# Optimization experiments

Measured on AMD Instinct MI355X. Metric: run time of the kernel, lower is better.

## Reference

```python
import jax, jax.numpy as jnp
import numpy as np

B, S0, S1 = 4, 768, 256
T = S0 + S1
D0, D1 = 2048, 1024
N, K, H = 8, 1, 256  # num_heads, num_kv_heads, head_dim
G = N // K
BIG_NEG = -2.3819763e38


def _apply_rope(x, positions, max_wavelength=10000):
    # x: [B, L, Hn, Hd]; positions: [B, L] float32
    half = x.shape[-1] // 2
    freq_exponents = (2.0 / x.shape[-1]) * jnp.arange(half, dtype=jnp.float32)
    timescale = max_wavelength ** freq_exponents
    radians = positions[..., None] / timescale[None, None, :]   # [B, L, half]
    radians = radians[..., None, :]                             # [B, L, 1, half]
    sin, cos = jnp.sin(radians), jnp.cos(radians)
    x1, x2 = jnp.split(x, 2, axis=-1)
    res = jnp.concatenate([x1 * cos - x2 * sin, x2 * cos + x1 * sin], axis=-1)
    return res.astype(x.dtype)


def setup_inputs() -> dict:
    key = jax.random.key(0)
    ks = jax.random.split(key, 8)
    x0 = jax.random.normal(ks[0], (B, S0, D0), dtype=jnp.float32)
    x1 = jax.random.normal(ks[1], (B, S1, D1), dtype=jnp.float32)
    positions = jnp.broadcast_to(jnp.arange(T, dtype=jnp.float32), (B, T))
    # causal mask [B, 1, T, T]
    attn_mask = jnp.broadcast_to(jnp.tril(jnp.ones((T, T), dtype=bool)), (B, 1, T, T))
    # lecun_normal-style init: std = 1/sqrt(fan_in=width)
    q0_w = jax.random.normal(ks[2], (N, D0, H), dtype=jnp.float32) * (D0 ** -0.5)
    kv0_w = jax.random.normal(ks[3], (2, K, D0, H), dtype=jnp.float32) * (D0 ** -0.5)
    q1_w = jax.random.normal(ks[4], (N, D1, H), dtype=jnp.float32) * (D1 ** -0.5)
    kv1_w = jax.random.normal(ks[5], (2, K, D1, H), dtype=jnp.float32) * (D1 ** -0.5)
    o0_w = jax.random.normal(ks[6], (N, H, D0), dtype=jnp.float32) * ((N * H) ** -0.5)
    o1_w = jax.random.normal(ks[7], (N, H, D1), dtype=jnp.float32) * ((N * H) ** -0.5)
    return {"x0": x0, "x1": x1, "positions": positions, "attn_mask": attn_mask,
            "q0_w": q0_w, "kv0_w": kv0_w, "q1_w": q1_w, "kv1_w": kv1_w,
            "o0_w": o0_w, "o1_w": o1_w}


def reference(x0, x1, positions, attn_mask, q0_w, kv0_w, q1_w, kv1_w, o0_w, o1_w):
    dtype = x0.dtype
    # per-stream GQA projections (num_kv_heads != num_heads path)
    q_a = jnp.einsum('BTD,NDH->BTNH', x0, q0_w)
    kv_a = jnp.einsum('BSD,CKDH->CBSKH', x0, kv0_w)
    q_b = jnp.einsum('BTD,NDH->BTNH', x1, q1_w)
    kv_b = jnp.einsum('BSD,CKDH->CBSKH', x1, kv1_w)
    # concat streams along sequence
    q = jnp.concatenate([q_a, q_b], axis=1)                 # [B, T, N, H]
    k = jnp.concatenate([kv_a[0], kv_b[0]], axis=1)         # [B, T, K, H]
    v = jnp.concatenate([kv_a[1], kv_b[1]], axis=1)         # [B, T, K, H]
    # inline RoPE + query scaling
    q = _apply_rope(q, positions) * (H ** -0.5)
    k = _apply_rope(k, positions)
    # GQA grouping: N = K * G
    qg = q.reshape(q.shape[0], q.shape[1], K, G, H)          # [B, T, K, G, H]
    logits = jnp.einsum('BTKGH,BSKH->BKGTS', qg, k,
                        preferred_element_type=jnp.float32)  # fp32 scores
    masked = jnp.where(attn_mask[:, :, None, :, :], logits, BIG_NEG)
    probs = jax.nn.softmax(masked, axis=-1).astype(dtype)
    encoded = jnp.einsum('BKGTS,BSKH->BTKGH', probs, v)
    encoded = encoded.reshape(encoded.shape[0], encoded.shape[1], N, H)  # [B, T, N, H]
    out0 = jnp.einsum('BTNH,NHD->BTD', encoded[:, :S0], o0_w)
    out1 = jnp.einsum('BTNH,NHD->BTD', encoded[:, S0:], o1_w)
    return (out0, out1)
```

## Files before the change

### kernel.cpp

```cpp
#include <hip/hip_runtime.h>

typedef unsigned short u16;
typedef __attribute__((ext_vector_type(8))) short bf16x8;
typedef __attribute__((ext_vector_type(4))) float f32x4;

#define CB   4
#define CS0  768
#define CS1  256
#define CT   1024
#define CD0  2048
#define CD1  1024
#define CN   8
#define CH   256
#define IDENT (1 << 30)
#define BIGBASE 0x7fffffff

__device__ __forceinline__ float bf2f(u16 u) {
    union { unsigned int i; float f; } v;
    v.i = ((unsigned int)u) << 16;
    return v.f;
}
__device__ __forceinline__ u16 f2bf(float f) {
    union { float f; unsigned int i; } v;
    v.f = f;
    unsigned int r = 0x7fffu + ((v.i >> 16) & 1u);
    return (u16)((v.i + r) >> 16);
}

__device__ __forceinline__ void gl_lds16(const u16* g, u16* lds_base) {
    __builtin_amdgcn_global_load_lds(
        (const __attribute__((address_space(1))) void*)g,
        (__attribute__((address_space(3))) void*)lds_base,
        16, 0, 0);
}

struct PSeg { const float* in; u16* out; int R, C, base, lgx, lgy, mode; };
struct PSeg8 { PSeg t[8]; };

__global__ __launch_bounds__(256) void prep_multi(PSeg8 segs)
{
    __shared__ float tl[32][33];
    int bid = blockIdx.x;
    PSeg g = segs.t[0];
    #pragma unroll
    for (int i = 1; i < 8; i++)
        if (bid >= segs.t[i].base) g = segs.t[i];
    int r = bid - g.base;
    if (g.mode == 0) {
        int i = r * 256 + threadIdx.x;
        float4 v = ((const float4*)g.in)[i];
        ushort4 o;
        o.x = f2bf(v.x); o.y = f2bf(v.y); o.z = f2bf(v.z); o.w = f2bf(v.w);
        ((ushort4*)g.out)[i] = o;
    } else {
        int bx = r & ((1 << g.lgx) - 1);
        int by = (r >> g.lgx) & ((1 << g.lgy) - 1);
        int bz = r >> (g.lgx + g.lgy);
        const float* in = g.in + (size_t)bz * g.R * g.C;
        u16* out = g.out + (size_t)bz * g.R * g.C;
        int c0 = bx * 32, r0 = by * 32;
        int tx = threadIdx.x & 31, ty = threadIdx.x >> 5;
        #pragma unroll
        for (int i = 0; i < 32; i += 8)
            tl[ty + i][tx] = in[(size_t)(r0 + ty + i) * g.C + c0 + tx];
        __syncthreads();
        #pragma unroll
        for (int i = 0; i < 32; i += 8)
            out[(size_t)(c0 + ty + i) * g.R + r0 + tx] = f2bf(tl[tx][ty + i]);
    }
}

struct GSeg {
    const u16* A; const u16* BT; void* C;
    int K, Cstride, base, lgnx;
    int Sa, Ta, ta, Sc, Tc, tc, obf, pad;
};
struct GSeg4 { GSeg s[4]; };

__global__ __launch_bounds__(256, 3) void gemm128_multi(GSeg4 segs)
{
    __shared__ __align__(16) u16 lds[3 * 8192];

    int bid = blockIdx.x;
    GSeg g = segs.s[0];
    if (bid >= segs.s[1].base) g = segs.s[1];
    if (bid >= segs.s[2].base) g = segs.s[2];
    if (bid >= segs.s[3].base) g = segs.s[3];

    int tid  = threadIdx.x;
    int r    = bid - g.base;
    int n0   = (r & ((1 << g.lgnx) - 1)) * 128;
    int m0   = (r >> g.lgnx) * 128;
    int wave = tid >> 6, lane = tid & 63;

    int srow  = tid >> 2;
    int skoff = ((tid & 3) ^ ((srow >> 1) & 3)) * 8;
    int am1 = m0 + srow, am2 = m0 + 64 + srow;
    const u16* aptr1 = g.A + (size_t)((am1 / g.Sa) * g.Ta + g.ta + am1 % g.Sa) * g.K + skoff;
    const u16* aptr2 = g.A + (size_t)((am2 / g.Sa) * g.Ta + g.ta + am2 % g.Sa) * g.K + skoff;
    const u16* bptr1 = g.BT + (size_t)(n0 + srow) * g.K + skoff;
    const u16* bptr2 = g.BT + (size_t)(n0 + 64 + srow) * g.K + skoff;

    int mw = (wave >> 1) * 64, nw = (wave & 1) * 64;
    int l15 = lane & 15;
    int q4  = lane >> 4;
    int sw  = (q4 ^ ((l15 >> 1) & 3)) * 8;

#define STAGE(bufi, tt) do { int kk = (tt) * 32; \
        u16* base = lds + (bufi) * 8192 + wave * 512; \
        gl_lds16(aptr1 + kk, base); \
        gl_lds16(aptr2 + kk, base + 2048); \
        gl_lds16(bptr1 + kk, base + 4096); \
        gl_lds16(bptr2 + kk, base + 6144); } while (0)

    f32x4 acc[4][4] = {};
    int nkt = g.K >> 5;

    STAGE(0, 0);
    STAGE(1, 1);

    int cur = 0, nxt = 2;
    for (int t = 0; t < nkt; ++t) {
        if (t + 1 < nkt) asm volatile("s_waitcnt vmcnt(4)" ::: "memory");
        else             asm volatile("s_waitcnt vmcnt(0)" ::: "memory");
        __builtin_amdgcn_sched_barrier(0);
        __builtin_amdgcn_s_barrier();
        asm volatile("" ::: "memory");
        if (t + 2 < nkt) STAGE(nxt, t + 2);

        const u16* At = lds + cur * 8192;
        const u16* Bt = At + 4096;
        bf16x8 af[4], bfr[4];
        #pragma unroll
        for (int i = 0; i < 4; i++)
            af[i] = *(const bf16x8*)&At[(mw + i * 16 + l15) * 32 + sw];
        #pragma unroll
        for (int i = 0; i < 4; i++)
            bfr[i] = *(const bf16x8*)&Bt[(nw + i * 16 + l15) * 32 + sw];
        asm volatile("s_waitcnt lgkmcnt(0)" ::: "memory");
        __builtin_amdgcn_sched_barrier(0);
        __builtin_amdgcn_s_setprio(1);
        #pragma unroll
        for (int mi = 0; mi < 4; mi++)
            #pragma unroll
            for (int ni = 0; ni < 4; ni++)
                acc[mi][ni] = __builtin_amdgcn_mfma_f32_16x16x32_bf16(
                    af[mi], bfr[ni], acc[mi][ni], 0, 0, 0);
        __builtin_amdgcn_s_setprio(0);
        cur = (cur == 2) ? 0 : cur + 1;
        nxt = (nxt == 2) ? 0 : nxt + 1;
    }
#undef STAGE

    #pragma unroll
    for (int mi = 0; mi < 4; mi++) {
        #pragma unroll
        for (int rr = 0; rr < 4; rr++) {
            int mm = m0 + mw + mi * 16 + q4 * 4 + rr;
            int grow = (mm / g.Sc) * g.Tc + g.tc + mm % g.Sc;
            if (g.obf) {
                u16* crow = (u16*)g.C + (size_t)grow * g.Cstride + n0 + nw + l15;
                #pragma unroll
                for (int ni = 0; ni < 4; ni++)
                    crow[ni * 16] = f2bf(acc[mi][ni][rr]);
            } else {
                float* crow = (float*)g.C + (size_t)grow * g.Cstride + n0 + nw + l15;
                #pragma unroll
                for (int ni = 0; ni < 4; ni++)
                    crow[ni * 16] = acc[mi][ni][rr];
            }
        }
    }
}

__global__ __launch_bounds__(256) void rope_vt_kernel(
    const u16* __restrict__ qsrc, const u16* __restrict__ kvsrc,
    const float* __restrict__ positions,
    u16* __restrict__ qb, u16* __restrict__ kb, u16* __restrict__ vto)
{
    int bid = blockIdx.x;
    if (bid < 18432) {
        int idx = bid * 256 + threadIdx.x;
        const int QP = CB * CT * CN * 128;
        if (idx < QP) {
            int h  = idx & 127;
            int n  = (idx >> 7) & 7;
            int bt = idx >> 10;
            const u16* base = qsrc + (size_t)bt * 2048 + n * 256;
            float pos = positions[bt];
            float ts  = powf(10000.0f, (float)h * (1.0f / 128.0f));
            float rr  = pos / ts;
            float sn = sinf(rr), cs = cosf(rr);
            float x1 = bf2f(base[h]), x2 = bf2f(base[h + 128]);
            u16* ob = qb + (size_t)bt * 2048 + n * 256;
            ob[h]       = f2bf((x1 * cs - x2 * sn) * 0.0625f);
            ob[h + 128] = f2bf((x2 * cs + x1 * sn) * 0.0625f);
        } else {
            int j  = idx - QP;
            int h  = j & 127;
            int bt = j >> 7;
            const u16* base = kvsrc + (size_t)bt * 512;
            float pos = positions[bt];
            float ts  = powf(10000.0f, (float)h * (1.0f / 128.0f));
            float rr  = pos / ts;
            float sn = sinf(rr), cs = cosf(rr);
            float x1 = bf2f(base[h]), x2 = bf2f(base[h + 128]);
            int b = bt >> 10, t = bt & 1023;
            int h2 = h + 128;
            kb[((size_t)(b * 8 + (h  >> 5)) * 1024 + t) * 32 + (h  & 31)] = f2bf(x1 * cs - x2 * sn);
            kb[((size_t)(b * 8 + (h2 >> 5)) * 1024 + t) * 32 + (h2 & 31)] = f2bf(x2 * cs + x1 * sn);
        }
    } else {
        int vb = bid - 18432;
        int h  = threadIdx.x;
        int sc = vb & 31;
        int b  = vb >> 5;
        const u16* src = kvsrc + ((size_t)(b * 1024 + sc * 32) * 512 + 256 + h);
        u16* dst = vto + ((size_t)(b * 32 + sc) * 256 + h) * 32;
        u16 buf[32];
        #pragma unroll
        for (int ss = 0; ss < 32; ss++)
            buf[ss] = src[(size_t)ss * 512];
        #pragma unroll
        for (int i = 0; i < 8; i++)
            ((ushort4*)dst)[i] = ((ushort4*)buf)[i];
    }
}

__global__ __launch_bounds__(256) void flash_attn(
    const u16* __restrict__ qb, const u16* __restrict__ kb,
    const u16* __restrict__ vt, u16* __restrict__ encoded)
{
    __shared__ __align__(16) u16 Ks[2 * 8192];
    __shared__ __align__(16) u16 Vs[2 * 8192];
    __shared__ __align__(16) u16 Pw[4][640];

    int tid  = threadIdx.x;
    int wave = tid >> 6, lane = tid & 63;
    int q4 = lane >> 4, l15 = lane & 15;
    int swz = (q4 ^ ((l15 >> 1) & 3)) * 8;

    int bid  = blockIdx.x;
    int half = bid >> 8;
    int r    = bid & 255;
    int b    = (half << 1) | (r >> 7);
    int ti   = r & 127;
    if (half) ti = 127 - ti;
    int t0 = ti * 8;

    bf16x8 af[8];
    {
        int m = wave * 16 + l15;
        int head = m >> 3, tl = m & 7;
        const u16* qrow = qb + ((size_t)(b * CT + t0 + tl) * 2048 + head * 256 + q4 * 8);
        #pragma unroll
        for (int kc = 0; kc < 8; kc++)
            af[kc] = *(const bf16x8*)(qrow + kc * 32);
    }

#define STAGE_KV(tt, bb) do { int ss0 = (tt) * 32; \
        _Pragma("unroll") \
        for (int is = 0; is < 4; ++is) { \
            int ubase = is * 256 + wave * 64; \
            int u = ubase + lane; \
            int gK = u & 3, sK = (u >> 2) & 31, hc = u >> 7; \
            int ug = gK ^ ((sK >> 1) & 3); \
            const u16* gp = kb + ((size_t)((b * 8 + hc) * 1024 + ss0 + sK) * 32 + ug * 8); \
            gl_lds16(gp, Ks + (bb) * 8192 + ubase * 8); \
        } \
        _Pragma("unroll") \
        for (int is = 0; is < 4; ++is) { \
            int ubase = is * 256 + wave * 64; \
            int u = ubase + lane; \
            int gV = u & 3, hv = u >> 2; \
            int vg = gV ^ ((hv >> 1) & 3); \
            const u16* gp = vt + ((size_t)(b * 32 + (ss0 >> 5)) * 8192 + (size_t)hv * 32 + vg * 8); \
            gl_lds16(gp, Vs + (bb) * 8192 + ubase * 8); \
        } } while (0)

    f32x4 O[16] = {};
    float lrun[4] = {0.f, 0.f, 0.f, 0.f};

    int send = t0 + 8;
    int nt   = (send + 31) >> 5;

    STAGE_KV(0, 0);

    for (int t = 0; t < nt; ++t) {
        asm volatile("s_waitcnt vmcnt(0)" ::: "memory");
        __builtin_amdgcn_sched_barrier(0);
        __builtin_amdgcn_s_barrier();
        asm volatile("" ::: "memory");
        if (t + 1 < nt) STAGE_KV(t + 1, (t + 1) & 1);

        const u16* Kb = Ks + (t & 1) * 8192;
        const u16* Vb = Vs + (t & 1) * 8192;
        int s0 = t * 32;

        f32x4 P[2];
        #pragma unroll
        for (int ni = 0; ni < 2; ni++) {
            f32x4 c = {};
            #pragma unroll
            for (int kc = 0; kc < 8; kc++) {
                bf16x8 bfr = *(const bf16x8*)&Kb[kc * 1024 + (ni * 16 + l15) * 32 + swz];
                c = __builtin_amdgcn_mfma_f32_16x16x32_bf16(af[kc], bfr, c, 0, 0, 0);
            }
            P[ni] = c;
        }

        if (t == nt - 1) {
            #pragma unroll
            for (int ni = 0; ni < 2; ni++)
                #pragma unroll
                for (int rr = 0; rr < 4; rr++) {
                    int trow = t0 + ((q4 * 4 + rr) & 7);
                    int scol = s0 + ni * 16 + l15;
                    if (scol > trow) P[ni][rr] = -3.0e38f;
                }
        }

        #pragma unroll
        for (int ni = 0; ni < 2; ni++)
            #pragma unroll
            for (int rr = 0; rr < 4; rr++) {
                float e = __expf(P[ni][rr]);
                P[ni][rr] = e;
                Pw[wave][(q4 * 4 + rr) * 40 + ni * 16 + l15] = f2bf(e);
            }
        #pragma unroll
        for (int rr = 0; rr < 4; rr++) {
            float s = P[0][rr] + P[1][rr];
            s += __shfl_xor(s, 1);
            s += __shfl_xor(s, 2);
            s += __shfl_xor(s, 4);
            s += __shfl_xor(s, 8);
            lrun[rr] += s;
        }

        bf16x8 pa = *(const bf16x8*)&Pw[wave][l15 * 40 + q4 * 8];
        #pragma unroll
        for (int nc = 0; nc < 16; nc++) {
            bf16x8 b0 = *(const bf16x8*)&Vb[(nc * 16 + l15) * 32 + swz];
            O[nc] = __builtin_amdgcn_mfma_f32_16x16x32_bf16(pa, b0, O[nc], 0, 0, 0);
        }
    }
#undef STAGE_KV

    #pragma unroll
    for (int rr = 0; rr < 4; rr++) {
        int mm = wave * 16 + q4 * 4 + rr;
        int hd = mm >> 3, tl = mm & 7;
        u16* erow = encoded + ((size_t)(b * CT + t0 + tl) * 2048 + hd * 256 + l15);
        float inv = 1.0f / lrun[rr];
        #pragma unroll
        for (int nc = 0; nc < 16; nc++)
            erow[nc * 16] = f2bf(O[nc][rr] * inv);
    }
}

extern "C" void kernel_launch(void* const* d_in, const int* in_sizes, int n_in,
                              void* d_out, int out_size, void* d_ws, size_t ws_size,
                              hipStream_t stream)
{
    const float* x0        = (const float*)d_in[0];
    const float* x1        = (const float*)d_in[1];
    const float* positions = (const float*)d_in[2];
    const float* q0_w  = (const float*)d_in[4];
    const float* kv0_w = (const float*)d_in[5];
    const float* q1_w  = (const float*)d_in[6];
    const float* kv1_w = (const float*)d_in[7];
    const float* o0_w  = (const float*)d_in[8];
    const float* o1_w  = (const float*)d_in[9];
    float* out = (float*)d_out;

    char* W = (char*)d_ws;
    u16* qbuf16  = (u16*)(W);
    u16* kvbuf16 = (u16*)(W + 16777216);
    u16* WTo0  = (u16*)(W + 20971520);
    u16* WTo1  = (u16*)(W + 29360128);
    u16* x0b   = (u16*)(W + 33554432);
    u16* x1b   = (u16*)(W + 46137344);
    u16* WTq0  = (u16*)(W + 48234496);
    u16* WTkv0 = (u16*)(W + 56623104);
    u16* WTq1  = (u16*)(W + 58720256);
    u16* WTkv1 = (u16*)(W + 62914560);
    u16* qb  = x0b;
    u16* kb  = WTkv0;
    u16* vtb = WTq1;
    u16* encoded = qbuf16;

    PSeg8 ps8;
    ps8.t[0] = { x0,    x0b,      0,    0,     0, 0, 0, 0 };
    ps8.t[1] = { x1,    x1b,      0,    0,  6144, 0, 0, 0 };
    ps8.t[2] = { q0_w,  WTq0,  2048,  256,  7168, 3, 6, 1 };
    ps8.t[3] = { kv0_w, WTkv0, 2048,  256, 11264, 3, 6, 1 };
    ps8.t[4] = { q1_w,  WTq1,  1024,  256, 12288, 3, 5, 1 };
    ps8.t[5] = { kv1_w, WTkv1, 1024,  256, 14336, 3, 5, 1 };
    ps8.t[6] = { o0_w,  WTo0,  2048, 2048, 14848, 6, 6, 1 };
    ps8.t[7] = { o1_w,  WTo1,  2048, 1024, 18944, 5, 6, 1 };
    prep_multi<<<dim3(20992), dim3(256), 0, stream>>>(ps8);

    GSeg4 ps;
    ps.s[0] = { x0b, WTq0,  qbuf16,  2048, 2048,   0, 4, IDENT, 0, 0, CS0, CT, 0,   1, 0 };
    ps.s[1] = { x0b, WTkv0, kvbuf16, 2048,  512, 384, 2, IDENT, 0, 0, CS0, CT, 0,   1, 0 };
    ps.s[2] = { x1b, WTq1,  qbuf16,  1024, 2048, 480, 4, IDENT, 0, 0, CS1, CT, CS0, 1, 0 };
    ps.s[3] = { x1b, WTkv1, kvbuf16, 1024,  512, 608, 2, IDENT, 0, 0, CS1, CT, CS0, 1, 0 };
    gemm128_multi<<<dim3(640), dim3(256), 0, stream>>>(ps);

    rope_vt_kernel<<<dim3(18560), dim3(256), 0, stream>>>(
        qbuf16, kvbuf16, positions, qb, kb, vtb);

    flash_attn<<<dim3(512), dim3(256), 0, stream>>>(qb, kb, vtb, encoded);

    GSeg4 os;
    os.s[0] = { encoded, WTo0, out, 2048, 2048,   0, 4, CS0, CT, 0,   IDENT, 0, 0, 0, 0 };
    os.s[1] = { encoded, WTo1, out + (size_t)CB * CS0 * CD0,
                2048, 1024, 384, 3, CS1, CT, CS0, IDENT, 0, 0, 0, 0 };
    os.s[2] = { nullptr, nullptr, nullptr, 128, 0, BIGBASE, 0, 1, 0, 0, 1, 0, 0, 0, 0 };
    os.s[3] = { nullptr, nullptr, nullptr, 128, 0, BIGBASE, 0, 1, 0, 0, 1, 0, 0, 0, 0 };
    gemm128_multi<<<dim3(448), dim3(256), 0, stream>>>(os);
}
```

Baseline: 311.1 us.

## Halve flash-attention block to four query rows and drop K/V double buffering

The attention kernel now launches 1024 blocks of two waves, each covering 4 query positions across all 8 heads instead of 8 positions across four waves. Row-to-head mapping and the causal-mask row index are adjusted to match. LDS K/V staging becomes single-buffered with two `__syncthreads` per key tile, replacing the prefetch of the next tile. The goal is more blocks and higher occupancy from the smaller LDS footprint. The cost is that each K/V tile is loaded into LDS by twice as many blocks, and load latency is no longer overlapped with MFMA work.

```diff
diff --git a/kernel.cpp b/kernel.cpp
--- a/kernel.cpp
+++ b/kernel.cpp
@@ -227,13 +227,13 @@
     }
 }
 
-__global__ __launch_bounds__(256) void flash_attn(
+__global__ __launch_bounds__(128) void flash_attn(
     const u16* __restrict__ qb, const u16* __restrict__ kb,
     const u16* __restrict__ vt, u16* __restrict__ encoded)
 {
-    __shared__ __align__(16) u16 Ks[2 * 8192];
-    __shared__ __align__(16) u16 Vs[2 * 8192];
-    __shared__ __align__(16) u16 Pw[4][640];
+    __shared__ __align__(16) u16 Ks[8192];
+    __shared__ __align__(16) u16 Vs[8192];
+    __shared__ __align__(16) u16 Pw[2][640];
 
     int tid  = threadIdx.x;
     int wave = tid >> 6, lane = tid & 63;
@@ -241,61 +241,51 @@
     int swz = (q4 ^ ((l15 >> 1) & 3)) * 8;
 
     int bid  = blockIdx.x;
-    int half = bid >> 8;
-    int r    = bid & 255;
-    int b    = (half << 1) | (r >> 7);
-    int ti   = r & 127;
-    if (half) ti = 127 - ti;
-    int t0 = ti * 8;
+    int half = bid >> 9;
+    int r    = bid & 511;
+    int b    = (half << 1) | (r >> 8);
+    int qi   = r & 255;
+    if (half) qi = 255 - qi;
+    int t0 = qi * 4;
 
     bf16x8 af[8];
     {
         int m = wave * 16 + l15;
-        int head = m >> 3, tl = m & 7;
+        int head = m >> 2, tl = m & 3;
         const u16* qrow = qb + ((size_t)(b * CT + t0 + tl) * 2048 + head * 256 + q4 * 8);
         #pragma unroll
         for (int kc = 0; kc < 8; kc++)
             af[kc] = *(const bf16x8*)(qrow + kc * 32);
     }
 
-#define STAGE_KV(tt, bb) do { int ss0 = (tt) * 32; \
-        _Pragma("unroll") \
-        for (int is = 0; is < 4; ++is) { \
-            int ubase = is * 256 + wave * 64; \
-            int u = ubase + lane; \
-            int gK = u & 3, sK = (u >> 2) & 31, hc = u >> 7; \
-            int ug = gK ^ ((sK >> 1) & 3); \
-            const u16* gp = kb + ((size_t)((b * 8 + hc) * 1024 + ss0 + sK) * 32 + ug * 8); \
-            gl_lds16(gp, Ks + (bb) * 8192 + ubase * 8); \
-        } \
-        _Pragma("unroll") \
-        for (int is = 0; is < 4; ++is) { \
-            int ubase = is * 256 + wave * 64; \
-            int u = ubase + lane; \
-            int gV = u & 3, hv = u >> 2; \
-            int vg = gV ^ ((hv >> 1) & 3); \
-            const u16* gp = vt + ((size_t)(b * 32 + (ss0 >> 5)) * 8192 + (size_t)hv * 32 + vg * 8); \
-            gl_lds16(gp, Vs + (bb) * 8192 + ubase * 8); \
-        } } while (0)
-
     f32x4 O[16] = {};
     float lrun[4] = {0.f, 0.f, 0.f, 0.f};
 
-    int send = t0 + 8;
+    int send = t0 + 4;
     int nt   = (send + 31) >> 5;
 
-    STAGE_KV(0, 0);
-
     for (int t = 0; t < nt; ++t) {
-        asm volatile("s_waitcnt vmcnt(0)" ::: "memory");
-        __builtin_amdgcn_sched_barrier(0);
-        __builtin_amdgcn_s_barrier();
-        asm volatile("" ::: "memory");
-        if (t + 1 < nt) STAGE_KV(t + 1, (t + 1) & 1);
-
-        const u16* Kb = Ks + (t & 1) * 8192;
-        const u16* Vb = Vs + (t & 1) * 8192;
         int s0 = t * 32;
+        if (t) __syncthreads();
+        #pragma unroll
+        for (int is = 0; is < 8; ++is) {
+            int ubase = is * 128 + wave * 64;
+            int u = ubase + lane;
+            int gK = u & 3, sK = (u >> 2) & 31, hc = u >> 7;
+            int ug = gK ^ ((sK >> 1) & 3);
+            const u16* gp = kb + ((size_t)((b * 8 + hc) * 1024 + s0 + sK) * 32 + ug * 8);
+            gl_lds16(gp, Ks + (size_t)ubase * 8);
+        }
+        #pragma unroll
+        for (int is = 0; is < 8; ++is) {
+            int ubase = is * 128 + wave * 64;
+            int u = ubase + lane;
+            int gV = u & 3, hv = u >> 2;
+            int vg = gV ^ ((hv >> 1) & 3);
+            const u16* gp = vt + ((size_t)(b * 32 + (s0 >> 5)) * 8192 + (size_t)hv * 32 + vg * 8);
+            gl_lds16(gp, Vs + (size_t)ubase * 8);
+        }
+        __syncthreads();
 
         f32x4 P[2];
         #pragma unroll
@@ -303,7 +293,7 @@
             f32x4 c = {};
             #pragma unroll
             for (int kc = 0; kc < 8; kc++) {
-                bf16x8 bfr = *(const bf16x8*)&Kb[kc * 1024 + (ni * 16 + l15) * 32 + swz];
+                bf16x8 bfr = *(const bf16x8*)&Ks[kc * 1024 + (ni * 16 + l15) * 32 + swz];
                 c = __builtin_amdgcn_mfma_f32_16x16x32_bf16(af[kc], bfr, c, 0, 0, 0);
             }
             P[ni] = c;
@@ -314,7 +304,7 @@
             for (int ni = 0; ni < 2; ni++)
                 #pragma unroll
                 for (int rr = 0; rr < 4; rr++) {
-                    int trow = t0 + ((q4 * 4 + rr) & 7);
+                    int trow = t0 + rr;
                     int scol = s0 + ni * 16 + l15;
                     if (scol > trow) P[ni][rr] = -3.0e38f;
                 }
@@ -341,16 +331,15 @@
         bf16x8 pa = *(const bf16x8*)&Pw[wave][l15 * 40 + q4 * 8];
         #pragma unroll
         for (int nc = 0; nc < 16; nc++) {
-            bf16x8 b0 = *(const bf16x8*)&Vb[(nc * 16 + l15) * 32 + swz];
+            bf16x8 b0 = *(const bf16x8*)&Vs[(nc * 16 + l15) * 32 + swz];
             O[nc] = __builtin_amdgcn_mfma_f32_16x16x32_bf16(pa, b0, O[nc], 0, 0, 0);
         }
     }
-#undef STAGE_KV
 
     #pragma unroll
     for (int rr = 0; rr < 4; rr++) {
         int mm = wave * 16 + q4 * 4 + rr;
-        int hd = mm >> 3, tl = mm & 7;
+        int hd = mm >> 2, tl = mm & 3;
         u16* erow = encoded + ((size_t)(b * CT + t0 + tl) * 2048 + hd * 256 + l15);
         float inv = 1.0f / lrun[rr];
         #pragma unroll
@@ -411,7 +400,7 @@
     rope_vt_kernel<<<dim3(18560), dim3(256), 0, stream>>>(
         qbuf16, kvbuf16, positions, qb, kb, vtb);
 
-    flash_attn<<<dim3(512), dim3(256), 0, stream>>>(qb, kb, vtb, encoded);
+    flash_attn<<<dim3(1024), dim3(128), 0, stream>>>(qb, kb, vtb, encoded);
 
     GSeg4 os;
     os.s[0] = { encoded, WTo0, out, 2048, 2048,   0, 4, CS0, CT, 0,   IDENT, 0, 0, 0, 0 };
```

After: 314.4 us. Within noise of the previous version (+1.1%).

## Shrink flash-attention blocks to two waves, each handling paired causal query tiles

Applied to the files above, without the earlier changes.

The flash attention kernel now uses 128-thread blocks with two waves and 4-query-row tiles. Each block processes two tiles in sequence, one near the start and its mirror near the end of the causal range, so work per block is balanced. s_setprio is raised around the MFMA loops to favour matrix issue over other waves. The change trades fewer rows per K/V staging (more total K/V traffic per query) for more, better-balanced blocks and higher occupancy.

```diff
diff --git a/kernel.cpp b/kernel.cpp
--- a/kernel.cpp
+++ b/kernel.cpp
@@ -227,136 +227,141 @@
     }
 }
 
-__global__ __launch_bounds__(256) void flash_attn(
+__global__ __launch_bounds__(128) void flash_attn(
     const u16* __restrict__ qb, const u16* __restrict__ kb,
     const u16* __restrict__ vt, u16* __restrict__ encoded)
 {
     __shared__ __align__(16) u16 Ks[2 * 8192];
     __shared__ __align__(16) u16 Vs[2 * 8192];
-    __shared__ __align__(16) u16 Pw[4][640];
+    __shared__ __align__(16) u16 Pw[2][640];
 
     int tid  = threadIdx.x;
     int wave = tid >> 6, lane = tid & 63;
     int q4 = lane >> 4, l15 = lane & 15;
     int swz = (q4 ^ ((l15 >> 1) & 3)) * 8;
 
-    int bid  = blockIdx.x;
-    int half = bid >> 8;
-    int r    = bid & 255;
-    int b    = (half << 1) | (r >> 7);
-    int ti   = r & 127;
-    if (half) ti = 127 - ti;
-    int t0 = ti * 8;
-
-    bf16x8 af[8];
-    {
-        int m = wave * 16 + l15;
-        int head = m >> 3, tl = m & 7;
-        const u16* qrow = qb + ((size_t)(b * CT + t0 + tl) * 2048 + head * 256 + q4 * 8);
-        #pragma unroll
-        for (int kc = 0; kc < 8; kc++)
-            af[kc] = *(const bf16x8*)(qrow + kc * 32);
-    }
-
-#define STAGE_KV(tt, bb) do { int ss0 = (tt) * 32; \
+    int bid = blockIdx.x;
+    int b   = bid >> 7;
+    int r   = bid & 127;
+
+#define STAGE_KV(ss0, bb) do { \
         _Pragma("unroll") \
-        for (int is = 0; is < 4; ++is) { \
-            int ubase = is * 256 + wave * 64; \
+        for (int is = 0; is < 8; ++is) { \
+            int ubase = is * 128 + wave * 64; \
             int u = ubase + lane; \
             int gK = u & 3, sK = (u >> 2) & 31, hc = u >> 7; \
             int ug = gK ^ ((sK >> 1) & 3); \
-            const u16* gp = kb + ((size_t)((b * 8 + hc) * 1024 + ss0 + sK) * 32 + ug * 8); \
-            gl_lds16(gp, Ks + (bb) * 8192 + ubase * 8); \
+            const u16* gp = kb + ((size_t)((b * 8 + hc) * 1024 + (ss0) + sK) * 32 + ug * 8); \
+            gl_lds16(gp, Ks + (bb) * 8192 + (size_t)ubase * 8); \
         } \
         _Pragma("unroll") \
-        for (int is = 0; is < 4; ++is) { \
-            int ubase = is * 256 + wave * 64; \
+        for (int is = 0; is < 8; ++is) { \
+            int ubase = is * 128 + wave * 64; \
             int u = ubase + lane; \
             int gV = u & 3, hv = u >> 2; \
             int vg = gV ^ ((hv >> 1) & 3); \
-            const u16* gp = vt + ((size_t)(b * 32 + (ss0 >> 5)) * 8192 + (size_t)hv * 32 + vg * 8); \
-            gl_lds16(gp, Vs + (bb) * 8192 + ubase * 8); \
+            const u16* gp = vt + ((size_t)(b * 32 + ((ss0) >> 5)) * 8192 + (size_t)hv * 32 + vg * 8); \
+            gl_lds16(gp, Vs + (bb) * 8192 + (size_t)ubase * 8); \
         } } while (0)
 
-    f32x4 O[16] = {};
-    float lrun[4] = {0.f, 0.f, 0.f, 0.f};
-
-    int send = t0 + 8;
-    int nt   = (send + 31) >> 5;
-
-    STAGE_KV(0, 0);
-
-    for (int t = 0; t < nt; ++t) {
-        asm volatile("s_waitcnt vmcnt(0)" ::: "memory");
-        __builtin_amdgcn_sched_barrier(0);
-        __builtin_amdgcn_s_barrier();
-        asm volatile("" ::: "memory");
-        if (t + 1 < nt) STAGE_KV(t + 1, (t + 1) & 1);
-
-        const u16* Kb = Ks + (t & 1) * 8192;
-        const u16* Vb = Vs + (t & 1) * 8192;
-        int s0 = t * 32;
-
-        f32x4 P[2];
-        #pragma unroll
-        for (int ni = 0; ni < 2; ni++) {
-            f32x4 c = {};
-            #pragma unroll
-            for (int kc = 0; kc < 8; kc++) {
-                bf16x8 bfr = *(const bf16x8*)&Kb[kc * 1024 + (ni * 16 + l15) * 32 + swz];
-                c = __builtin_amdgcn_mfma_f32_16x16x32_bf16(af[kc], bfr, c, 0, 0, 0);
+    #pragma unroll 1
+    for (int ph = 0; ph < 2; ++ph) {
+        int qc = ph ? (255 - r) : r;
+        int t0 = qc * 4;
+        int nt = (t0 + 4 + 31) >> 5;
+
+        bf16x8 af[8];
+        {
+            int m = wave * 16 + l15;
+            int head = m >> 2, tl = m & 3;
+            const u16* qrow = qb + ((size_t)(b * CT + t0 + tl) * 2048 + head * 256 + q4 * 8);
+            #pragma unroll
+            for (int kc = 0; kc < 8; kc++)
+                af[kc] = *(const bf16x8*)(qrow + kc * 32);
+        }
+
+        f32x4 O[16] = {};
+        float lrun[4] = {0.f, 0.f, 0.f, 0.f};
+
+        __syncthreads();
+        STAGE_KV(0, 0);
+
+        for (int t = 0; t < nt; ++t) {
+            asm volatile("s_waitcnt vmcnt(0)" ::: "memory");
+            __builtin_amdgcn_sched_barrier(0);
+            __builtin_amdgcn_s_barrier();
+            asm volatile("" ::: "memory");
+            if (t + 1 < nt) STAGE_KV((t + 1) * 32, (t + 1) & 1);
+
+            const u16* Kb = Ks + (t & 1) * 8192;
+            const u16* Vb = Vs + (t & 1) * 8192;
+            int s0 = t * 32;
+
+            f32x4 P[2];
+            #pragma unroll
+            for (int ni = 0; ni < 2; ni++) {
+                f32x4 c = {};
+                __builtin_amdgcn_s_setprio(1);
+                #pragma unroll
+                for (int kc = 0; kc < 8; kc++) {
+                    bf16x8 bfr = *(const bf16x8*)&Kb[kc * 1024 + (ni * 16 + l15) * 32 + swz];
+                    c = __builtin_amdgcn_mfma_f32_16x16x32_bf16(af[kc], bfr, c, 0, 0, 0);
+                }
+                __builtin_amdgcn_s_setprio(0);
+                P[ni] = c;
             }
-            P[ni] = c;
-        }
-
-        if (t == nt - 1) {
+
+            if (t == nt - 1) {
+                #pragma unroll
+                for (int ni = 0; ni < 2; ni++)
+                    #pragma unroll
+                    for (int rr = 0; rr < 4; rr++) {
+                        int trow = t0 + rr;
+                        int scol = s0 + ni * 16 + l15;
+                        if (scol > trow) P[ni][rr] = -3.0e38f;
+                    }
+            }
+
             #pragma unroll
             for (int ni = 0; ni < 2; ni++)
                 #pragma unroll
                 for (int rr = 0; rr < 4; rr++) {
-                    int trow = t0 + ((q4 * 4 + rr) & 7);
-                    int scol = s0 + ni * 16 + l15;
-                    if (scol > trow) P[ni][rr] = -3.0e38f;
+                    float e = __expf(P[ni][rr]);
+                    P[ni][rr] = e;
+                    Pw[wave][(q4 * 4 + rr) * 40 + ni * 16 + l15] = f2bf(e);
                 }
+            #pragma unroll
+            for (int rr = 0; rr < 4; rr++) {
+                float s = P[0][rr] + P[1][rr];
+                s += __shfl_xor(s, 1);
+                s += __shfl_xor(s, 2);
+                s += __shfl_xor(s, 4);
+                s += __shfl_xor(s, 8);
+                lrun[rr] += s;
+            }
+
+            bf16x8 pa = *(const bf16x8*)&Pw[wave][l15 * 40 + q4 * 8];
+            __builtin_amdgcn_s_setprio(1);
+            #pragma unroll
+            for (int nc = 0; nc < 16; nc++) {
+                bf16x8 b0 = *(const bf16x8*)&Vb[(nc * 16 + l15) * 32 + swz];
+                O[nc] = __builtin_amdgcn_mfma_f32_16x16x32_bf16(pa, b0, O[nc], 0, 0, 0);
+            }
+            __builtin_amdgcn_s_setprio(0);
         }
 
         #pragma unroll
-        for (int ni = 0; ni < 2; ni++)
-            #pragma unroll
-            for (int rr = 0; rr < 4; rr++) {
-                float e = __expf(P[ni][rr]);
-                P[ni][rr] = e;
-                Pw[wave][(q4 * 4 + rr) * 40 + ni * 16 + l15] = f2bf(e);
-            }
-        #pragma unroll
         for (int rr = 0; rr < 4; rr++) {
-            float s = P[0][rr] + P[1][rr];
-            s += __shfl_xor(s, 1);
-            s += __shfl_xor(s, 2);
-            s += __shfl_xor(s, 4);
-            s += __shfl_xor(s, 8);
-            lrun[rr] += s;
-        }
-
-        bf16x8 pa = *(const bf16x8*)&Pw[wave][l15 * 40 + q4 * 8];
-        #pragma unroll
-        for (int nc = 0; nc < 16; nc++) {
-            bf16x8 b0 = *(const bf16x8*)&Vb[(nc * 16 + l15) * 32 + swz];
-            O[nc] = __builtin_amdgcn_mfma_f32_16x16x32_bf16(pa, b0, O[nc], 0, 0, 0);
+            int mm = wave * 16 + q4 * 4 + rr;
+            int hd = mm >> 2, tl = mm & 3;
+            u16* erow = encoded + ((size_t)(b * CT + t0 + tl) * 2048 + hd * 256 + l15);
+            float inv = 1.0f / lrun[rr];
+            #pragma unroll
+            for (int nc = 0; nc < 16; nc++)
+                erow[nc * 16] = f2bf(O[nc][rr] * inv);
         }
     }
 #undef STAGE_KV
-
-    #pragma unroll
-    for (int rr = 0; rr < 4; rr++) {
-        int mm = wave * 16 + q4 * 4 + rr;
-        int hd = mm >> 3, tl = mm & 7;
-        u16* erow = encoded + ((size_t)(b * CT + t0 + tl) * 2048 + hd * 256 + l15);
-        float inv = 1.0f / lrun[rr];
-        #pragma unroll
-        for (int nc = 0; nc < 16; nc++)
-            erow[nc * 16] = f2bf(O[nc][rr] * inv);
-    }
 }
 
 extern "C" void kernel_launch(void* const* d_in, const int* in_sizes, int n_in,
@@ -411,7 +416,7 @@
     rope_vt_kernel<<<dim3(18560), dim3(256), 0, stream>>>(
         qbuf16, kvbuf16, positions, qb, kb, vtb);
 
-    flash_attn<<<dim3(512), dim3(256), 0, stream>>>(qb, kb, vtb, encoded);
+    flash_attn<<<dim3(512), dim3(128), 0, stream>>>(qb, kb, vtb, encoded);
 
     GSeg4 os;
     os.s[0] = { encoded, WTo0, out, 2048, 2048,   0, 4, CS0, CT, 0,   IDENT, 0, 0, 0, 0 };
```

Result: slower. 321.2 us (+3.3%).
